# Optimization experiments

Measured on AMD Instinct MI355X. Metric: run time of the kernel, lower is better.

Reference implementation:

```python
import jax, jax.numpy as jnp
import numpy as np

B, S, DM, H, DF = 2, 2048, 1024, 16, 4096
HD = DM // H
EPS = 1e-6
NEG = -1e9


def setup_inputs() -> dict:
    key = jax.random.key(0)
    ks = jax.random.split(key, 16)
    sc = 1.0 / np.sqrt(DM)
    scf = 1.0 / np.sqrt(DF)
    return {
        "x": jax.random.normal(ks[0], (B, S, DM), jnp.float32),
        "src_mask": jax.random.randint(ks[1], (B, 1, 1, S), 0, 2, jnp.int32),
        "Wq": jax.random.normal(ks[2], (DM, DM), jnp.float32) * sc,
        "bq": jnp.zeros((DM,), jnp.float32),
        "Wk": jax.random.normal(ks[3], (DM, DM), jnp.float32) * sc,
        "bk": jnp.zeros((DM,), jnp.float32),
        "Wv": jax.random.normal(ks[4], (DM, DM), jnp.float32) * sc,
        "bv": jnp.zeros((DM,), jnp.float32),
        "Wo": jax.random.normal(ks[5], (DM, DM), jnp.float32) * sc,
        "bo": jnp.zeros((DM,), jnp.float32),
        "W1": jax.random.normal(ks[6], (DM, DF), jnp.float32) * sc,
        "b1": jnp.zeros((DF,), jnp.float32),
        "W2": jax.random.normal(ks[7], (DF, DM), jnp.float32) * scf,
        "b2": jnp.zeros((DM,), jnp.float32),
        "alpha1": jnp.ones((1,), jnp.float32),
        "beta1": jnp.ones((1,), jnp.float32),
        "alpha2": jnp.ones((1,), jnp.float32),
        "beta2": jnp.ones((1,), jnp.float32),
    }


def layer_norm(x, alpha, beta):
    # torch: mean + unbiased std (ddof=1), scalar alpha/beta, eps added to std
    mean = jnp.mean(x, axis=-1, keepdims=True)
    std = jnp.std(x, axis=-1, keepdims=True, ddof=1)
    return alpha * (x - mean) / (std + EPS) + beta


def mha(x, mask, Wq, bq, Wk, bk, Wv, bv, Wo, bo):
    def split(t):  # [B,S,DM] -> [B,H,S,HD]
        return t.reshape(B, S, H, HD).transpose(0, 2, 1, 3)
    q = split(x @ Wq + bq)
    k = split(x @ Wk + bk)
    v = split(x @ Wv + bv)
    scores = jnp.einsum("bhqd,bhkd->bhqk", q, k) / np.sqrt(HD)
    scores = jnp.where(mask == 0, NEG, scores)
    probs = jax.nn.softmax(scores, axis=-1)  # dropout in eval mode = identity
    out = jnp.einsum("bhqk,bhkd->bhqd", probs, v)
    out = out.transpose(0, 2, 1, 3).reshape(B, S, DM)
    return out @ Wo + bo


def reference(x, src_mask, Wq, bq, Wk, bk, Wv, bv, Wo, bo, W1, b1, W2, b2,
              alpha1, beta1, alpha2, beta2):
    # pre-norm residual: x + attn(norm(x)); dropout disabled (eval)
    n1 = layer_norm(x, alpha1, beta1)
    h = x + mha(n1, src_mask, Wq, bq, Wk, bk, Wv, bv, Wo, bo)
    n2 = layer_norm(h, alpha2, beta2)
    ff = jax.nn.relu(n2 @ W1 + b1) @ W2 + b2
    return h + ff
```

## Files before the change

### kernel.cpp

```cpp
#include <hip/hip_runtime.h>
#include <hip/hip_bf16.h>

#define SEQ   2048
#define BATCH 2
#define DMODEL 1024
#define DFF   4096
#define NHEAD 16
#define HDIM  64
#define NTOK  (BATCH*SEQ)

typedef short s8v __attribute__((ext_vector_type(8)));
typedef float f4v __attribute__((ext_vector_type(4)));

__device__ __forceinline__ float b2f(unsigned short u) {
    union { unsigned int i; float f; } v; v.i = ((unsigned int)u) << 16; return v.f;
}
__device__ __forceinline__ unsigned short f2b(float f) {
    union { unsigned int i; float f; } v; v.f = f;
    unsigned int r = v.i + 0x7FFFu + ((v.i >> 16) & 1u);
    return (unsigned short)(r >> 16);
}
__device__ __forceinline__ ushort2 cvt_pk(float a, float b) {
    __hip_bfloat162 h = __float22bfloat162_rn(float2{ a, b });
    return *(ushort2*)&h;
}

__device__ __forceinline__ f4v mfma_bf16(s8v a, s8v b, f4v c) {
    return __builtin_amdgcn_mfma_f32_16x16x32_bf16(a, b, c, 0, 0, 0);
}

__device__ __forceinline__ void gload_lds16(const void* g, void* l) {
    __builtin_amdgcn_global_load_lds(
        (const __attribute__((address_space(1))) unsigned int*)g,
        (__attribute__((address_space(3))) unsigned int*)l, 16, 0, 0);
}

template<int N> __device__ __forceinline__ void wait_vmcnt() {
    if constexpr (N == 8)      asm volatile("s_waitcnt vmcnt(8)" ::: "memory");
    else if constexpr (N == 6) asm volatile("s_waitcnt vmcnt(6)" ::: "memory");
    else if constexpr (N == 2) asm volatile("s_waitcnt vmcnt(2)" ::: "memory");
    else                       asm volatile("s_waitcnt vmcnt(0)" ::: "memory");
}

__device__ __forceinline__ void tp_tile(const float* __restrict__ src,
                                        unsigned short* __restrict__ dst,
                                        int R, int C, int br, int bc, int t,
                                        unsigned short* tl) {
    for (int i = 0; i < 16; i++) {
        int idx = t + 256 * i;
        int r = idx >> 6, c = idx & 63;
        tl[r * 65 + c] = f2b(src[(size_t)(br * 64 + r) * C + bc * 64 + c]);
    }
    __syncthreads();
    for (int i = 0; i < 16; i++) {
        int idx = t + 256 * i;
        int r2 = idx >> 6, c2 = idx & 63;
        dst[(size_t)(bc * 64 + r2) * R + br * 64 + c2] = tl[c2 * 65 + r2];
    }
}

__global__ __launch_bounds__(256) void prep_weights(const float* __restrict__ Wq,
                                                    const float* __restrict__ Wk,
                                                    const float* __restrict__ Wv,
                                                    const float* __restrict__ Wo,
                                                    const float* __restrict__ W1,
                                                    const float* __restrict__ W2,
                                                    const float* __restrict__ bq,
                                                    const float* __restrict__ bk,
                                                    const float* __restrict__ bv,
                                                    const float* __restrict__ x,
                                                    const float* __restrict__ a1,
                                                    const float* __restrict__ be1,
                                                    unsigned short* __restrict__ Wqkv_t,
                                                    unsigned short* __restrict__ Wo_t,
                                                    unsigned short* __restrict__ W1_t,
                                                    unsigned short* __restrict__ W2_t,
                                                    float* __restrict__ bqkv,
                                                    unsigned short* __restrict__ n1) {
    __shared__ unsigned short tl[64 * 65];
    __shared__ float red[8];
    const int t = threadIdx.x;
    const int bx = blockIdx.x, by = blockIdx.y, z = blockIdx.z;
    if (z < 4) {
        const float* src = (z == 0) ? Wq : (z == 1) ? Wk : (z == 2) ? Wv : Wo;
        unsigned short* dst = (z == 3) ? Wo_t : Wqkv_t + (size_t)z * 1024 * 1024;
        tp_tile(src, dst, 1024, 1024, bx, by, t, tl);
    } else if (z == 4) {
        for (int i = 0; i < 4; i++) {
            tp_tile(W1, W1_t, 1024, 4096, bx, by + 16 * i, t, tl);
            __syncthreads();
        }
    } else if (z == 5) {
        if (bx == 0 && by == 0) {
            for (int i = 0; i < 12; i++) {
                int idx = t + 256 * i;
                if (idx < 1024) bqkv[idx] = bq[idx];
                else if (idx < 2048) bqkv[idx] = bk[idx - 1024];
                else if (idx < 3072) bqkv[idx] = bv[idx - 2048];
            }
        }
        for (int i = 0; i < 4; i++) {
            tp_tile(W2, W2_t, 4096, 1024, bx + 16 * i, by, t, tl);
            __syncthreads();
        }
    } else {
        const int row = (z - 6) * 256 + by * 16 + bx;
        const float* xr = x + (size_t)row * DMODEL;
        float4 u = ((const float4*)xr)[t];
        float v[4] = { u.x, u.y, u.z, u.w };
        float s = v[0] + v[1] + v[2] + v[3];
        float sq = v[0]*v[0] + v[1]*v[1] + v[2]*v[2] + v[3]*v[3];
        for (int off = 32; off; off >>= 1) { s += __shfl_xor(s, off); sq += __shfl_xor(sq, off); }
        int wave = t >> 6, lane = t & 63;
        if (!lane) { red[wave] = s; red[4 + wave] = sq; }
        __syncthreads();
        s = red[0] + red[1] + red[2] + red[3];
        sq = red[4] + red[5] + red[6] + red[7];
        float mean = s * (1.f / DMODEL);
        float var = (sq - (float)DMODEL * mean * mean) * (1.f / (DMODEL - 1));
        var = var < 0.f ? 0.f : var;
        float inv = a1[0] / (sqrtf(var) + 1e-6f);
        float bt = be1[0];
        uint2 ou;
        unsigned short r0 = f2b((v[0] - mean) * inv + bt);
        unsigned short r1 = f2b((v[1] - mean) * inv + bt);
        unsigned short r2 = f2b((v[2] - mean) * inv + bt);
        unsigned short r3 = f2b((v[3] - mean) * inv + bt);
        ou.x = (unsigned int)r0 | ((unsigned int)r1 << 16);
        ou.y = (unsigned int)r2 | ((unsigned int)r3 << 16);
        ((uint2*)(n1 + (size_t)row * DMODEL))[t] = ou;
    }
}

__global__ __launch_bounds__(256) void mask_scan(const int* __restrict__ msk,
                                                 int* __restrict__ idx,
                                                 float* __restrict__ maskc2,
                                                 int* __restrict__ ntiles) {
    const int b = blockIdx.x, t = threadIdx.x;
    const int base = b * SEQ;
    __shared__ int wsum[4];
    int k[8]; int cnt = 0;
    for (int j = 0; j < 8; j++) {
        k[j] = (msk[base + t * 8 + j] != 0) ? 1 : 0;
        cnt += k[j];
    }
    const int lane = t & 63, wv = t >> 6;
    int pre = cnt;
    for (int off = 1; off < 64; off <<= 1) {
        int n = __shfl_up(pre, off);
        if (lane >= off) pre += n;
    }
    if (lane == 63) wsum[wv] = pre;
    __syncthreads();
    const int Nb = wsum[0] + wsum[1] + wsum[2] + wsum[3];
    int woff = 0;
    for (int w = 0; w < wv; w++) woff += wsum[w];
    const int excl = woff + pre - cnt;
    for (int j = 0; j < 8; j++) {
        int g = t * 8 + j;
        idx[base + g] = 0;
        maskc2[base + g] = (g < Nb) ? 0.f : -1e9f;
    }
    __syncthreads();
    int pos = excl;
    for (int j = 0; j < 8; j++) {
        if (k[j]) { idx[base + pos] = t * 8 + j; pos++; }
    }
    if (t == 0) ntiles[b] = (Nb + 63) >> 6;
}

__global__ __launch_bounds__(256) void pack_kv(const unsigned short* __restrict__ Kb,
                                               const unsigned short* __restrict__ Vb,
                                               const int* __restrict__ idx,
                                               const int* __restrict__ ntiles,
                                               unsigned short* __restrict__ Kc,
                                               unsigned short* __restrict__ Vc) {
    __shared__ unsigned short tl[64 * 65];
    const int t = threadIdx.x;
    const int kt = blockIdx.x, h = blockIdx.y, b = blockIdx.z;
    if (kt >= ntiles[b]) return;
    const int* idxb = idx + b * SEQ + kt * 64;
    const unsigned short* srcK = Kb + (size_t)b * SEQ * 1024 + h * HDIM;
    unsigned short* dstK = Kc + ((size_t)((b * NHEAD + h) * 32 + kt)) * 4096;
    for (int i = 0; i < 2; i++) {
        int ci = t + 256 * i;
        int r = ci >> 3, cp = ci & 7;
        int cl = cp ^ (r & 7);
        int row = idxb[r];
        *(uint4*)&dstK[ci * 8] = *(const uint4*)&srcK[(size_t)row * 1024 + cl * 8];
    }
    const unsigned short* srcV = Vb + (size_t)b * SEQ * 1024 + h * HDIM;
    for (int i = 0; i < 16; i++) {
        int idx2 = t + 256 * i;
        int r = idx2 >> 6, c = idx2 & 63;
        int row = idxb[r];
        tl[r * 65 + c] = srcV[(size_t)row * 1024 + c];
    }
    __syncthreads();
    unsigned short* dstV = Vc + ((size_t)((b * NHEAD + h) * 32 + kt)) * 4096;
    for (int i = 0; i < 2; i++) {
        int ci = t + 256 * i;
        int r = ci >> 3, cp = ci & 7;
        int cl = cp ^ (r & 7);
        ushort4 e0, e1;
        e0.x = tl[(cl * 8 + 0) * 65 + r]; e0.y = tl[(cl * 8 + 1) * 65 + r];
        e0.z = tl[(cl * 8 + 2) * 65 + r]; e0.w = tl[(cl * 8 + 3) * 65 + r];
        e1.x = tl[(cl * 8 + 4) * 65 + r]; e1.y = tl[(cl * 8 + 5) * 65 + r];
        e1.z = tl[(cl * 8 + 6) * 65 + r]; e1.w = tl[(cl * 8 + 7) * 65 + r];
        *(ushort4*)&dstV[ci * 8]     = e0;
        *(ushort4*)&dstV[ci * 8 + 4] = e1;
    }
}

__global__ __launch_bounds__(256) void ln_kernel(const float* __restrict__ x,
                                                 const float* __restrict__ al,
                                                 const float* __restrict__ be,
                                                 unsigned short* __restrict__ o) {
    const int row = blockIdx.x;
    const float* xr = x + (size_t)row * DMODEL;
    float4 u = ((const float4*)xr)[threadIdx.x];
    float v[4] = { u.x, u.y, u.z, u.w };
    float s = v[0] + v[1] + v[2] + v[3];
    float sq = v[0]*v[0] + v[1]*v[1] + v[2]*v[2] + v[3]*v[3];
    for (int off = 32; off; off >>= 1) { s += __shfl_xor(s, off); sq += __shfl_xor(sq, off); }
    __shared__ float red[8];
    int wave = threadIdx.x >> 6, lane = threadIdx.x & 63;
    if (!lane) { red[wave] = s; red[4 + wave] = sq; }
    __syncthreads();
    s = red[0] + red[1] + red[2] + red[3];
    sq = red[4] + red[5] + red[6] + red[7];
    float mean = s * (1.f / DMODEL);
    float var = (sq - (float)DMODEL * mean * mean) * (1.f / (DMODEL - 1));
    var = var < 0.f ? 0.f : var;
    float inv = al[0] / (sqrtf(var) + 1e-6f);
    float bt = be[0];
    uint2 ou;
    unsigned short r0 = f2b((v[0] - mean) * inv + bt);
    unsigned short r1 = f2b((v[1] - mean) * inv + bt);
    unsigned short r2 = f2b((v[2] - mean) * inv + bt);
    unsigned short r3 = f2b((v[3] - mean) * inv + bt);
    ou.x = (unsigned int)r0 | ((unsigned int)r1 << 16);
    ou.y = (unsigned int)r2 | ((unsigned int)r3 << 16);
    ((uint2*)(o + (size_t)row * DMODEL))[threadIdx.x] = ou;
}

template<int BROWS>
__device__ __forceinline__ void stage256(const unsigned short* __restrict__ A,
                                         const unsigned short* __restrict__ Bt,
                                         int m0, int n0, int K, int k0,
                                         unsigned short* sA, unsigned short* sB, int t) {
#pragma unroll
    for (int i = 0; i < 4; i++) {
        int ci = i * 512 + t;
        int r = ci >> 3, c = (ci & 7) ^ (r & 7);
        gload_lds16(A + (size_t)(m0 + r) * K + k0 + c * 8, sA + (size_t)ci * 8);
    }
#pragma unroll
    for (int i = 0; i < BROWS / 64; i++) {
        int ci = i * 512 + t;
        int r = ci >> 3, c = (ci & 7) ^ (r & 7);
        gload_lds16(Bt + (size_t)(n0 + r) * K + k0 + c * 8, sB + (size_t)ci * 8);
    }
}

template<int NFC>
__device__ __forceinline__ void comp256(const unsigned short* sA, const unsigned short* sB,
                                        int wm, int wn, int l16, int quad,
                                        f4v acc[8][NFC]) {
#pragma unroll
    for (int s = 0; s < 2; s++) {
        s8v b[NFC];
#pragma unroll
        for (int ni = 0; ni < NFC; ni++) {
            int r = wn * (NFC * 16) + ni * 16 + l16;
            int p = (s * 4 + quad) ^ (r & 7);
            b[ni] = *(const s8v*)&sB[r * 64 + p * 8];
        }
#pragma unroll
        for (int mi = 0; mi < 8; mi++) {
            int r = wm * 128 + mi * 16 + l16;
            int p = (s * 4 + quad) ^ (r & 7);
            s8v a = *(const s8v*)&sA[r * 64 + p * 8];
#pragma unroll
            for (int ni = 0; ni < NFC; ni++)
                acc[mi][ni] = mfma_bf16(a, b[ni], acc[mi][ni]);
        }
    }
}

template<bool RELU, bool RES, typename CT, bool SPLIT3, int BN>
__global__ __launch_bounds__(512, 2) void gemm256(const unsigned short* __restrict__ A,
                                                  const unsigned short* __restrict__ Bt,
                                                  const float* __restrict__ bias,
                                                  const float* __restrict__ res,
                                                  CT* __restrict__ C,
                                                  float* __restrict__ pbuf,
                                                  int M, int N, int K, int KS) {
    constexpr int NFC = BN / 64;
    constexpr int LPT = 4 + BN / 64;
    __shared__ __align__(16) unsigned short smA[2][256 * 64];
    __shared__ __align__(16) unsigned short smB[2][BN * 64];
    const int t = threadIdx.x;
    const int wave = t >> 6, lane = t & 63;
    const int quad = lane >> 4, l16 = lane & 15;
    const int wm = wave >> 2, wn = wave & 3;
    const int m0 = blockIdx.x * 256, n0 = blockIdx.y * BN;
    const int z = blockIdx.z;
    const int kbeg = z * KS;
    const int nt = KS >> 6;

    f4v acc[8][NFC] = {};

    stage256<BN>(A, Bt, m0, n0, K, kbeg,      smA[0], smB[0], t);
    stage256<BN>(A, Bt, m0, n0, K, kbeg + 64, smA[1], smB[1], t);
    wait_vmcnt<LPT>();
    __builtin_amdgcn_s_barrier();

    for (int it = 0; it < nt - 2; ++it) {
        const int cb = it & 1;
        __builtin_amdgcn_s_setprio(1);
        comp256<NFC>(smA[cb], smB[cb], wm, wn, l16, quad, acc);
        __builtin_amdgcn_s_setprio(0);
        asm volatile("s_waitcnt lgkmcnt(0)" ::: "memory");
        __builtin_amdgcn_s_barrier();
        stage256<BN>(A, Bt, m0, n0, K, kbeg + (it + 2) * 64, smA[cb], smB[cb], t);
        wait_vmcnt<LPT>();
        __builtin_amdgcn_s_barrier();
    }
    {
        const int cb = (nt - 2) & 1;
        __builtin_amdgcn_s_setprio(1);
        comp256<NFC>(smA[cb], smB[cb], wm, wn, l16, quad, acc);
        __builtin_amdgcn_s_setprio(0);
        asm volatile("s_waitcnt vmcnt(0)" ::: "memory");
        __builtin_amdgcn_s_barrier();
    }
    {
        const int cb = (nt - 1) & 1;
        __builtin_amdgcn_s_setprio(1);
        comp256<NFC>(smA[cb], smB[cb], wm, wn, l16, quad, acc);
        __builtin_amdgcn_s_setprio(0);
    }

#pragma unroll
    for (int mi = 0; mi < 8; mi++) {
#pragma unroll
        for (int ni = 0; ni < NFC; ni++) {
            const int col = n0 + wn * (NFC * 16) + ni * 16 + l16;
            const int row0 = m0 + wm * 128 + mi * 16 + quad * 4;
            if (z == 0) {
                const float bv = bias[col];
#pragma unroll
                for (int r = 0; r < 4; r++) {
                    float v = acc[mi][ni][r] + bv;
                    if (RELU) v = v > 0.f ? v : 0.f;
                    if (RES) v += res[(size_t)(row0 + r) * N + col];
                    size_t cidx;
                    if constexpr (SPLIT3)
                        cidx = (size_t)(col >> 10) * ((size_t)NTOK * 1024)
                             + (size_t)(row0 + r) * 1024 + (col & 1023);
                    else
                        cidx = (size_t)(row0 + r) * N + col;
                    if constexpr (sizeof(CT) == 2)
                        C[cidx] = f2b(v);
                    else
                        C[cidx] = v;
                }
            } else {
#pragma unroll
                for (int r = 0; r < 4; r++)
                    pbuf[(size_t)(z - 1) * M * N + (size_t)(row0 + r) * N + col]
                        = acc[mi][ni][r];
            }
        }
    }
}

__global__ __launch_bounds__(256) void add_pbuf(float* __restrict__ out,
                                                const float* __restrict__ pbuf) {
    const int i0 = (blockIdx.x * 256 + threadIdx.x) * 8;
    float4 a0 = *(const float4*)&out[i0];
    float4 a1 = *(const float4*)&out[i0 + 4];
    float4 p0 = *(const float4*)&pbuf[i0];
    float4 p1 = *(const float4*)&pbuf[i0 + 4];
    a0.x += p0.x; a0.y += p0.y; a0.z += p0.z; a0.w += p0.w;
    a1.x += p1.x; a1.y += p1.y; a1.z += p1.z; a1.w += p1.w;
    *(float4*)&out[i0]     = a0;
    *(float4*)&out[i0 + 4] = a1;
}

#define EXPC 0.18033688f
__device__ __forceinline__ void attn_tile(const unsigned short* __restrict__ smKb,
                                          const unsigned short* __restrict__ smVb,
                                          const float* __restrict__ smM, int k0,
                                          unsigned short* __restrict__ smPw,
                                          s8v qf0, s8v qf1, int quad, int l16,
                                          float& l_s, f4v* oacc) {
    const int l7 = l16 & 7;
    f4v s[4];
#pragma unroll
    for (int kt4 = 0; kt4 < 4; kt4++) {
        int r = kt4 * 16 + l16;
        s8v kf0 = *(const s8v*)&smKb[r * 64 + ((quad ^ l7) * 8)];
        s8v kf1 = *(const s8v*)&smKb[r * 64 + (((quad + 4) ^ l7) * 8)];
        f4v z = {};
        z = mfma_bf16(kf0, qf0, z);
        z = mfma_bf16(kf1, qf1, z);
        s[kt4] = z;
    }
#pragma unroll
    for (int kt4 = 0; kt4 < 4; kt4++) {
        float4 mf = *(const float4*)&smM[k0 + kt4 * 16 + quad * 4];
        s[kt4][0] = s[kt4][0] * EXPC + mf.x;
        s[kt4][1] = s[kt4][1] * EXPC + mf.y;
        s[kt4][2] = s[kt4][2] * EXPC + mf.z;
        s[kt4][3] = s[kt4][3] * EXPC + mf.w;
    }
#pragma unroll
    for (int kt4 = 0; kt4 < 4; kt4++)
#pragma unroll
        for (int r = 0; r < 4; r++) {
            float p = __builtin_amdgcn_exp2f(s[kt4][r]);
            s[kt4][r] = p;
            l_s += p;
        }
#pragma unroll
    for (int kt4 = 0; kt4 < 4; kt4++) {
        ushort2 p01 = cvt_pk(s[kt4][0], s[kt4][1]);
        ushort2 p23 = cvt_pk(s[kt4][2], s[kt4][3]);
        ushort4 pk;
        pk.x = p01.x; pk.y = p01.y; pk.z = p23.x; pk.w = p23.y;
        int c = kt4 * 2 + (quad >> 1);
        *(ushort4*)&smPw[l16 * 64 + ((c ^ l7) * 8 + (quad & 1) * 4)] = pk;
    }
    s8v pf0 = *(const s8v*)&smPw[l16 * 64 + ((quad ^ l7) * 8)];
    s8v pf1 = *(const s8v*)&smPw[l16 * 64 + (((quad + 4) ^ l7) * 8)];
#pragma unroll
    for (int nt = 0; nt < 4; nt++) {
        int r = nt * 16 + l16;
        s8v v0 = *(const s8v*)&smVb[r * 64 + ((quad ^ l7) * 8)];
        s8v v1 = *(const s8v*)&smVb[r * 64 + (((quad + 4) ^ l7) * 8)];
        oacc[nt] = mfma_bf16(pf0, v0, oacc[nt]);
        oacc[nt] = mfma_bf16(pf1, v1, oacc[nt]);
    }
}

__global__ __launch_bounds__(512) void attn_kernel(const unsigned short* __restrict__ Qb,
                                                   const unsigned short* __restrict__ Kc,
                                                   const unsigned short* __restrict__ Vc,
                                                   const float* __restrict__ maskc2,
                                                   const int* __restrict__ ntiles,
                                                   unsigned short* __restrict__ out) {
    __shared__ __align__(16) unsigned short smK[2][4096];
    __shared__ __align__(16) unsigned short smV[2][4096];
    __shared__ __align__(16) unsigned short smP[8][1024];
    __shared__ __align__(16) float smM[SEQ];

    const int t = threadIdx.x;
    const int wave = t >> 6, lane = t & 63;
    const int quad = lane >> 4, l16 = lane & 15;
    const int qt = blockIdx.x, h = blockIdx.y, b = blockIdx.z;
    const int q0 = qt * 128 + wave * 16;
    const int nt = ntiles[b];
    const unsigned short* Kbh = Kc + ((size_t)(b * NHEAD + h)) * 32 * 4096;
    const unsigned short* Vbh = Vc + ((size_t)(b * NHEAD + h)) * 32 * 4096;
    unsigned short* smPw = &smP[wave][0];

    const unsigned short* Qp = Qb + ((size_t)b * SEQ + q0 + l16) * 1024 + h * HDIM + quad * 8;
    s8v qf0 = *(const s8v*)(Qp);
    s8v qf1 = *(const s8v*)(Qp + 32);

    gload_lds16(maskc2 + (size_t)b * SEQ + t * 4, (float*)smM + t * 4);
    gload_lds16(Kbh + t * 8,        smK[0] + t * 8);
    gload_lds16(Vbh + t * 8,        smV[0] + t * 8);
    gload_lds16(Kbh + 4096 + t * 8, smK[1] + t * 8);
    gload_lds16(Vbh + 4096 + t * 8, smV[1] + t * 8);
    wait_vmcnt<2>();
    __builtin_amdgcn_s_barrier();

    float l_s = 0.f;
    f4v oacc[4] = {};

    for (int it = 0; it < nt; ++it) {
        const int cb = it & 1;
        __builtin_amdgcn_s_setprio(1);
        attn_tile(smK[cb], smV[cb], smM, it * 64, smPw, qf0, qf1, quad, l16, l_s, oacc);
        __builtin_amdgcn_s_setprio(0);
        if (it + 2 < nt) {
            asm volatile("s_waitcnt lgkmcnt(0)" ::: "memory");
            __builtin_amdgcn_s_barrier();
            gload_lds16(Kbh + (size_t)(it + 2) * 4096 + t * 8, smK[cb] + t * 8);
            gload_lds16(Vbh + (size_t)(it + 2) * 4096 + t * 8, smV[cb] + t * 8);
            wait_vmcnt<2>();
            __builtin_amdgcn_s_barrier();
        } else if (it + 1 < nt) {
            asm volatile("s_waitcnt lgkmcnt(0)" ::: "memory");
            __builtin_amdgcn_s_barrier();
            wait_vmcnt<0>();
            __builtin_amdgcn_s_barrier();
        }
    }

    l_s += __shfl_xor(l_s, 16);
    l_s += __shfl_xor(l_s, 32);
    float lrr[4];
    for (int r = 0; r < 4; r++) lrr[r] = __shfl(l_s, quad * 4 + r);
    for (int nt2 = 0; nt2 < 4; nt2++)
        for (int r = 0; r < 4; r++) {
            int row = q0 + quad * 4 + r;
            int col = h * HDIM + nt2 * 16 + l16;
            out[((size_t)b * SEQ + row) * DMODEL + col] = f2b(oacc[nt2][r] / lrr[r]);
        }
}

extern "C" void kernel_launch(void* const* d_in, const int* in_sizes, int n_in,
                              void* d_out, int out_size, void* d_ws, size_t ws_size,
                              hipStream_t stream) {
    const float* x   = (const float*)d_in[0];
    const int*   msk = (const int*)d_in[1];
    const float* Wq  = (const float*)d_in[2];
    const float* bq  = (const float*)d_in[3];
    const float* Wk  = (const float*)d_in[4];
    const float* bk  = (const float*)d_in[5];
    const float* Wv  = (const float*)d_in[6];
    const float* bv  = (const float*)d_in[7];
    const float* Wo  = (const float*)d_in[8];
    const float* bo  = (const float*)d_in[9];
    const float* W1  = (const float*)d_in[10];
    const float* b1  = (const float*)d_in[11];
    const float* W2  = (const float*)d_in[12];
    const float* b2  = (const float*)d_in[13];
    const float* a1  = (const float*)d_in[14];
    const float* be1 = (const float*)d_in[15];
    const float* a2  = (const float*)d_in[16];
    const float* be2 = (const float*)d_in[17];
    float* outf = (float*)d_out;

    char* ws = (char*)d_ws;
    const size_t MB = 1024 * 1024;
    unsigned short* W2_t   = (unsigned short*)(ws);
    unsigned short* W1_t   = (unsigned short*)(ws + 8 * MB);
    float*          Pbuf   = (float*)(ws + 8 * MB);
    unsigned short* Wqkv_t = (unsigned short*)(ws + 16 * MB);
    float*          bqkv   = (float*)(ws + 22 * MB);
    unsigned short* Kc     = (unsigned short*)(ws + 16 * MB);
    unsigned short* n2     = (unsigned short*)(ws + 16 * MB);
    unsigned short* Wo_t   = (unsigned short*)(ws + 24 * MB);
    unsigned short* Qb     = (unsigned short*)(ws + 26 * MB);
    unsigned short* Kb     = (unsigned short*)(ws + 34 * MB);
    unsigned short* Vb     = (unsigned short*)(ws + 42 * MB);
    float*          Pbuf2  = (float*)(ws + 34 * MB);
    unsigned short* ff1    = (unsigned short*)(ws + 26 * MB);
    unsigned short* attnO  = (unsigned short*)(ws + 50 * MB);
    unsigned short* n1     = (unsigned short*)d_out;
    unsigned short* Vc     = (unsigned short*)d_out;
    float*          hbuf   = (float*)d_out;
    float*          maskc2 = (float*)((char*)d_out + 8 * MB);
    int*            idxc   = (int*)((char*)d_out + 8 * MB + 16 * 1024);
    int*            ntl    = (int*)((char*)d_out + 8 * MB + 32 * 1024);

    mask_scan<<<dim3(BATCH), 256, 0, stream>>>(msk, idxc, maskc2, ntl);
    prep_weights<<<dim3(16, 16, 22), 256, 0, stream>>>(
        Wq, Wk, Wv, Wo, W1, W2, bq, bk, bv, x, a1, be1,
        Wqkv_t, Wo_t, W1_t, W2_t, bqkv, n1);

    gemm256<false, false, unsigned short, true, 256><<<dim3(16, 12, 1), 512, 0, stream>>>(
        n1, Wqkv_t, bqkv, nullptr, Qb, nullptr, NTOK, 3072, 1024, 1024);
    pack_kv<<<dim3(32, 16, 2), 256, 0, stream>>>(Kb, Vb, idxc, ntl, Kc, Vc);
    attn_kernel<<<dim3(16, 16, 2), 512, 0, stream>>>(Qb, Kc, Vc, maskc2, ntl, attnO);
    gemm256<false, true, float, false, 128><<<dim3(16, 8, 2), 512, 0, stream>>>(
        attnO, Wo_t, bo, x, hbuf, Pbuf2, NTOK, 1024, 1024, 512);
    add_pbuf<<<dim3(2048), 256, 0, stream>>>(hbuf, Pbuf2);
    ln_kernel<<<NTOK, 256, 0, stream>>>(hbuf, a2, be2, n2);
    gemm256<true, false, unsigned short, false, 256><<<dim3(16, 16, 1), 512, 0, stream>>>(
        n2, W1_t, b1, nullptr, ff1, nullptr, NTOK, DFF, 1024, 1024);
    gemm256<false, true, float, false, 128><<<dim3(16, 8, 2), 512, 0, stream>>>(
        ff1, W2_t, b2, hbuf, outf, Pbuf, NTOK, 1024, 4096, 2048);
    add_pbuf<<<dim3(2048), 256, 0, stream>>>(outf, Pbuf);
}
```

Measured before the change: 353.1 us.

## Replace 256-row GEMMs with 128x128 intra-K-split kernel and fuse small launches

Replaces the 256-row GEMM with a 128x128-tile kernel in which two wave groups split each K-step and reduce their partial sums through LDS. Block order is swizzled for cache locality, and the attention grid is swizzled the same way. Mask scanning moves into the prep kernel and the split-K partial add merges into LayerNorm, cutting launches. Transpose tiles now use vectorized float4 loads and ushort4 stores. Smaller tiles raise occupancy and the block count, but lower per-tile data reuse and add an LDS reduction.

```diff
diff --git a/kernel.cpp b/kernel.cpp
--- a/kernel.cpp
+++ b/kernel.cpp
@@ -38,6 +38,7 @@
 template<int N> __device__ __forceinline__ void wait_vmcnt() {
     if constexpr (N == 8)      asm volatile("s_waitcnt vmcnt(8)" ::: "memory");
     else if constexpr (N == 6) asm volatile("s_waitcnt vmcnt(6)" ::: "memory");
+    else if constexpr (N == 4) asm volatile("s_waitcnt vmcnt(4)" ::: "memory");
     else if constexpr (N == 2) asm volatile("s_waitcnt vmcnt(2)" ::: "memory");
     else                       asm volatile("s_waitcnt vmcnt(0)" ::: "memory");
 }
@@ -46,16 +47,25 @@
                                         unsigned short* __restrict__ dst,
                                         int R, int C, int br, int bc, int t,
                                         unsigned short* tl) {
-    for (int i = 0; i < 16; i++) {
-        int idx = t + 256 * i;
-        int r = idx >> 6, c = idx & 63;
-        tl[r * 65 + c] = f2b(src[(size_t)(br * 64 + r) * C + bc * 64 + c]);
+    for (int i = 0; i < 4; i++) {
+        int lin = i * 1024 + t * 4;
+        int r = lin >> 6, c = lin & 63;
+        float4 u = *(const float4*)&src[(size_t)(br * 64 + r) * C + bc * 64 + c];
+        tl[r * 65 + c + 0] = f2b(u.x);
+        tl[r * 65 + c + 1] = f2b(u.y);
+        tl[r * 65 + c + 2] = f2b(u.z);
+        tl[r * 65 + c + 3] = f2b(u.w);
     }
     __syncthreads();
-    for (int i = 0; i < 16; i++) {
-        int idx = t + 256 * i;
-        int r2 = idx >> 6, c2 = idx & 63;
-        dst[(size_t)(bc * 64 + r2) * R + br * 64 + c2] = tl[c2 * 65 + r2];
+    for (int i = 0; i < 4; i++) {
+        int lin = i * 1024 + t * 4;
+        int r2 = lin >> 6, c2 = lin & 63;
+        ushort4 o;
+        o.x = tl[(c2 + 0) * 65 + r2];
+        o.y = tl[(c2 + 1) * 65 + r2];
+        o.z = tl[(c2 + 2) * 65 + r2];
+        o.w = tl[(c2 + 3) * 65 + r2];
+        *(ushort4*)&dst[(size_t)(bc * 64 + r2) * R + br * 64 + c2] = o;
     }
 }
 
@@ -71,14 +81,19 @@
                                                     const float* __restrict__ x,
                                                     const float* __restrict__ a1,
                                                     const float* __restrict__ be1,
+                                                    const int* __restrict__ msk,
                                                     unsigned short* __restrict__ Wqkv_t,
                                                     unsigned short* __restrict__ Wo_t,
                                                     unsigned short* __restrict__ W1_t,
                                                     unsigned short* __restrict__ W2_t,
                                                     float* __restrict__ bqkv,
-                                                    unsigned short* __restrict__ n1) {
+                                                    unsigned short* __restrict__ n1,
+                                                    int* __restrict__ idxc,
+                                                    float* __restrict__ maskc2,
+                                                    int* __restrict__ ntl) {
     __shared__ unsigned short tl[64 * 65];
     __shared__ float red[8];
+    __shared__ int wsum[4];
     const int t = threadIdx.x;
     const int bx = blockIdx.x, by = blockIdx.y, z = blockIdx.z;
     if (z < 4) {
@@ -103,6 +118,38 @@
             tp_tile(W2, W2_t, 4096, 1024, bx + 16 * i, by, t, tl);
             __syncthreads();
         }
+    } else if (z == 22) {
+        if (bx >= BATCH || by != 0) return;
+        const int b = bx;
+        const int base = b * SEQ;
+        int k[8]; int cnt = 0;
+        for (int j = 0; j < 8; j++) {
+            k[j] = (msk[base + t * 8 + j] != 0) ? 1 : 0;
+            cnt += k[j];
+        }
+        const int lane = t & 63, wv = t >> 6;
+        int pre = cnt;
+        for (int off = 1; off < 64; off <<= 1) {
+            int n = __shfl_up(pre, off);
+            if (lane >= off) pre += n;
+        }
+        if (lane == 63) wsum[wv] = pre;
+        __syncthreads();
+        const int Nb = wsum[0] + wsum[1] + wsum[2] + wsum[3];
+        int woff = 0;
+        for (int w = 0; w < wv; w++) woff += wsum[w];
+        const int excl = woff + pre - cnt;
+        for (int j = 0; j < 8; j++) {
+            int g = t * 8 + j;
+            idxc[base + g] = 0;
+            maskc2[base + g] = (g < Nb) ? 0.f : -1e9f;
+        }
+        __syncthreads();
+        int pos = excl;
+        for (int j = 0; j < 8; j++) {
+            if (k[j]) { idxc[base + pos] = t * 8 + j; pos++; }
+        }
+        if (t == 0) ntl[b] = (Nb + 63) >> 6;
     } else {
         const int row = (z - 6) * 256 + by * 16 + bx;
         const float* xr = x + (size_t)row * DMODEL;
@@ -132,43 +179,6 @@
     }
 }
 
-__global__ __launch_bounds__(256) void mask_scan(const int* __restrict__ msk,
-                                                 int* __restrict__ idx,
-                                                 float* __restrict__ maskc2,
-                                                 int* __restrict__ ntiles) {
-    const int b = blockIdx.x, t = threadIdx.x;
-    const int base = b * SEQ;
-    __shared__ int wsum[4];
-    int k[8]; int cnt = 0;
-    for (int j = 0; j < 8; j++) {
-        k[j] = (msk[base + t * 8 + j] != 0) ? 1 : 0;
-        cnt += k[j];
-    }
-    const int lane = t & 63, wv = t >> 6;
-    int pre = cnt;
-    for (int off = 1; off < 64; off <<= 1) {
-        int n = __shfl_up(pre, off);
-        if (lane >= off) pre += n;
-    }
-    if (lane == 63) wsum[wv] = pre;
-    __syncthreads();
-    const int Nb = wsum[0] + wsum[1] + wsum[2] + wsum[3];
-    int woff = 0;
-    for (int w = 0; w < wv; w++) woff += wsum[w];
-    const int excl = woff + pre - cnt;
-    for (int j = 0; j < 8; j++) {
-        int g = t * 8 + j;
-        idx[base + g] = 0;
-        maskc2[base + g] = (g < Nb) ? 0.f : -1e9f;
-    }
-    __syncthreads();
-    int pos = excl;
-    for (int j = 0; j < 8; j++) {
-        if (k[j]) { idx[base + pos] = t * 8 + j; pos++; }
-    }
-    if (t == 0) ntiles[b] = (Nb + 63) >> 6;
-}
-
 __global__ __launch_bounds__(256) void pack_kv(const unsigned short* __restrict__ Kb,
                                                const unsigned short* __restrict__ Vb,
                                                const int* __restrict__ idx,
@@ -212,13 +222,18 @@
     }
 }
 
-__global__ __launch_bounds__(256) void ln_kernel(const float* __restrict__ x,
-                                                 const float* __restrict__ al,
-                                                 const float* __restrict__ be,
-                                                 unsigned short* __restrict__ o) {
+__global__ __launch_bounds__(256) void ln_add(float* __restrict__ hb,
+                                              const float* __restrict__ pbuf,
+                                              const float* __restrict__ al,
+                                              const float* __restrict__ be,
+                                              unsigned short* __restrict__ o) {
     const int row = blockIdx.x;
-    const float* xr = x + (size_t)row * DMODEL;
-    float4 u = ((const float4*)xr)[threadIdx.x];
+    float* hr = hb + (size_t)row * DMODEL;
+    const float* pr = pbuf + (size_t)row * DMODEL;
+    float4 u = ((const float4*)hr)[threadIdx.x];
+    float4 p = ((const float4*)pr)[threadIdx.x];
+    u.x += p.x; u.y += p.y; u.z += p.z; u.w += p.w;
+    ((float4*)hr)[threadIdx.x] = u;
     float v[4] = { u.x, u.y, u.z, u.w };
     float s = v[0] + v[1] + v[2] + v[3];
     float sq = v[0]*v[0] + v[1]*v[1] + v[2]*v[2] + v[3]*v[3];
@@ -244,138 +259,6 @@
     ((uint2*)(o + (size_t)row * DMODEL))[threadIdx.x] = ou;
 }
 
-template<int BROWS>
-__device__ __forceinline__ void stage256(const unsigned short* __restrict__ A,
-                                         const unsigned short* __restrict__ Bt,
-                                         int m0, int n0, int K, int k0,
-                                         unsigned short* sA, unsigned short* sB, int t) {
-#pragma unroll
-    for (int i = 0; i < 4; i++) {
-        int ci = i * 512 + t;
-        int r = ci >> 3, c = (ci & 7) ^ (r & 7);
-        gload_lds16(A + (size_t)(m0 + r) * K + k0 + c * 8, sA + (size_t)ci * 8);
-    }
-#pragma unroll
-    for (int i = 0; i < BROWS / 64; i++) {
-        int ci = i * 512 + t;
-        int r = ci >> 3, c = (ci & 7) ^ (r & 7);
-        gload_lds16(Bt + (size_t)(n0 + r) * K + k0 + c * 8, sB + (size_t)ci * 8);
-    }
-}
-
-template<int NFC>
-__device__ __forceinline__ void comp256(const unsigned short* sA, const unsigned short* sB,
-                                        int wm, int wn, int l16, int quad,
-                                        f4v acc[8][NFC]) {
-#pragma unroll
-    for (int s = 0; s < 2; s++) {
-        s8v b[NFC];
-#pragma unroll
-        for (int ni = 0; ni < NFC; ni++) {
-            int r = wn * (NFC * 16) + ni * 16 + l16;
-            int p = (s * 4 + quad) ^ (r & 7);
-            b[ni] = *(const s8v*)&sB[r * 64 + p * 8];
-        }
-#pragma unroll
-        for (int mi = 0; mi < 8; mi++) {
-            int r = wm * 128 + mi * 16 + l16;
-            int p = (s * 4 + quad) ^ (r & 7);
-            s8v a = *(const s8v*)&sA[r * 64 + p * 8];
-#pragma unroll
-            for (int ni = 0; ni < NFC; ni++)
-                acc[mi][ni] = mfma_bf16(a, b[ni], acc[mi][ni]);
-        }
-    }
-}
-
-template<bool RELU, bool RES, typename CT, bool SPLIT3, int BN>
-__global__ __launch_bounds__(512, 2) void gemm256(const unsigned short* __restrict__ A,
-                                                  const unsigned short* __restrict__ Bt,
-                                                  const float* __restrict__ bias,
-                                                  const float* __restrict__ res,
-                                                  CT* __restrict__ C,
-                                                  float* __restrict__ pbuf,
-                                                  int M, int N, int K, int KS) {
-    constexpr int NFC = BN / 64;
-    constexpr int LPT = 4 + BN / 64;
-    __shared__ __align__(16) unsigned short smA[2][256 * 64];
-    __shared__ __align__(16) unsigned short smB[2][BN * 64];
-    const int t = threadIdx.x;
-    const int wave = t >> 6, lane = t & 63;
-    const int quad = lane >> 4, l16 = lane & 15;
-    const int wm = wave >> 2, wn = wave & 3;
-    const int m0 = blockIdx.x * 256, n0 = blockIdx.y * BN;
-    const int z = blockIdx.z;
-    const int kbeg = z * KS;
-    const int nt = KS >> 6;
-
-    f4v acc[8][NFC] = {};
-
-    stage256<BN>(A, Bt, m0, n0, K, kbeg,      smA[0], smB[0], t);
-    stage256<BN>(A, Bt, m0, n0, K, kbeg + 64, smA[1], smB[1], t);
-    wait_vmcnt<LPT>();
-    __builtin_amdgcn_s_barrier();
-
-    for (int it = 0; it < nt - 2; ++it) {
-        const int cb = it & 1;
-        __builtin_amdgcn_s_setprio(1);
-        comp256<NFC>(smA[cb], smB[cb], wm, wn, l16, quad, acc);
-        __builtin_amdgcn_s_setprio(0);
-        asm volatile("s_waitcnt lgkmcnt(0)" ::: "memory");
-        __builtin_amdgcn_s_barrier();
-        stage256<BN>(A, Bt, m0, n0, K, kbeg + (it + 2) * 64, smA[cb], smB[cb], t);
-        wait_vmcnt<LPT>();
-        __builtin_amdgcn_s_barrier();
-    }
-    {
-        const int cb = (nt - 2) & 1;
-        __builtin_amdgcn_s_setprio(1);
-        comp256<NFC>(smA[cb], smB[cb], wm, wn, l16, quad, acc);
-        __builtin_amdgcn_s_setprio(0);
-        asm volatile("s_waitcnt vmcnt(0)" ::: "memory");
-        __builtin_amdgcn_s_barrier();
-    }
-    {
-        const int cb = (nt - 1) & 1;
-        __builtin_amdgcn_s_setprio(1);
-        comp256<NFC>(smA[cb], smB[cb], wm, wn, l16, quad, acc);
-        __builtin_amdgcn_s_setprio(0);
-    }
-
-#pragma unroll
-    for (int mi = 0; mi < 8; mi++) {
-#pragma unroll
-        for (int ni = 0; ni < NFC; ni++) {
-            const int col = n0 + wn * (NFC * 16) + ni * 16 + l16;
-            const int row0 = m0 + wm * 128 + mi * 16 + quad * 4;
-            if (z == 0) {
-                const float bv = bias[col];
-#pragma unroll
-                for (int r = 0; r < 4; r++) {
-                    float v = acc[mi][ni][r] + bv;
-                    if (RELU) v = v > 0.f ? v : 0.f;
-                    if (RES) v += res[(size_t)(row0 + r) * N + col];
-                    size_t cidx;
-                    if constexpr (SPLIT3)
-                        cidx = (size_t)(col >> 10) * ((size_t)NTOK * 1024)
-                             + (size_t)(row0 + r) * 1024 + (col & 1023);
-                    else
-                        cidx = (size_t)(row0 + r) * N + col;
-                    if constexpr (sizeof(CT) == 2)
-                        C[cidx] = f2b(v);
-                    else
-                        C[cidx] = v;
-                }
-            } else {
-#pragma unroll
-                for (int r = 0; r < 4; r++)
-                    pbuf[(size_t)(z - 1) * M * N + (size_t)(row0 + r) * N + col]
-                        = acc[mi][ni][r];
-            }
-        }
-    }
-}
-
 __global__ __launch_bounds__(256) void add_pbuf(float* __restrict__ out,
                                                 const float* __restrict__ pbuf) {
     const int i0 = (blockIdx.x * 256 + threadIdx.x) * 8;
@@ -389,6 +272,141 @@
     *(float4*)&out[i0 + 4] = a1;
 }
 
+
+__device__ __forceinline__ void stage128(const unsigned short* __restrict__ mat,
+                                         int base, int K, int k0,
+                                         unsigned short* sdst, int t) {
+#pragma unroll
+    for (int q = 0; q < 2; q++) {
+        int rl = t >> 3;
+        int c  = (t & 7) ^ (rl & 7);
+        gload_lds16(mat + (size_t)(base + q * 64 + rl) * K + k0 + c * 8,
+                    sdst + q * 4096 + (size_t)t * 8);
+    }
+}
+
+__device__ __forceinline__ s8v rdfrag128(const unsigned short* sm, int q, int fi,
+                                         int l16, int quad, int sW) {
+    int rl = fi * 16 + l16;
+    int p = (sW * 4 + quad) ^ (l16 & 7);
+    return *(const s8v*)&sm[q * 4096 + rl * 64 + p * 8];
+}
+
+template<bool RELU, bool RES, bool SPLITK, bool SPLIT3, typename CT>
+__global__ __launch_bounds__(512, 4) void gemm128k(const unsigned short* __restrict__ A,
+                                                   const unsigned short* __restrict__ Bt,
+                                                   const float* __restrict__ bias,
+                                                   const float* __restrict__ res,
+                                                   CT* __restrict__ C,
+                                                   float* __restrict__ pbuf,
+                                                   int M, int N, int K, int KS) {
+    __shared__ __align__(16) unsigned short smem[4][8192];
+    const int t = threadIdx.x;
+    const int wave = t >> 6, lane = t & 63;
+    const int quad = lane >> 4, l16 = lane & 15;
+    const int sW = wave >> 2, wm = (wave >> 1) & 1, wn = wave & 1;
+    const int lin = blockIdx.x + blockIdx.y * gridDim.x;
+    const int cpx = (gridDim.x * gridDim.y) >> 3;
+    const int swz = (lin & 7) * cpx + (lin >> 3);
+    int z, m0, n0;
+    if constexpr (SPLITK) {
+        z  = swz & 1;
+        m0 = ((swz >> 1) & 31) * 128;
+        n0 = (swz >> 6) * 128;
+    } else {
+        z  = 0;
+        m0 = (swz & 31) * 128;
+        n0 = (swz >> 5) * 128;
+    }
+    const int kbeg = z * KS;
+    const int nt = KS >> 6;
+
+    f4v acc[4][4] = {};
+
+    stage128(A,  m0, K, kbeg,      smem[0], t);
+    stage128(Bt, n0, K, kbeg,      smem[2], t);
+    stage128(A,  m0, K, kbeg + 64, smem[1], t);
+    stage128(Bt, n0, K, kbeg + 64, smem[3], t);
+    wait_vmcnt<4>();
+    __builtin_amdgcn_s_barrier();
+
+    for (int it = 0; it < nt; ++it) {
+        const int cb = it & 1;
+        const unsigned short* sA = smem[cb];
+        const unsigned short* sB = smem[2 + cb];
+        s8v a[4], b[4];
+#pragma unroll
+        for (int i = 0; i < 4; i++) a[i] = rdfrag128(sA, wm, i, l16, quad, sW);
+#pragma unroll
+        for (int i = 0; i < 4; i++) b[i] = rdfrag128(sB, wn, i, l16, quad, sW);
+        __builtin_amdgcn_s_setprio(1);
+#pragma unroll
+        for (int mi = 0; mi < 4; mi++)
+#pragma unroll
+            for (int ni = 0; ni < 4; ni++)
+                acc[mi][ni] = mfma_bf16(a[mi], b[ni], acc[mi][ni]);
+        __builtin_amdgcn_s_setprio(0);
+        asm volatile("s_waitcnt lgkmcnt(0)" ::: "memory");
+        __builtin_amdgcn_s_barrier();
+        if (it + 2 < nt) {
+            stage128(A,  m0, K, kbeg + (it + 2) * 64, smem[cb], t);
+            stage128(Bt, n0, K, kbeg + (it + 2) * 64, smem[2 + cb], t);
+            wait_vmcnt<4>();
+        } else if (it + 1 < nt) {
+            wait_vmcnt<0>();
+        }
+        __builtin_amdgcn_s_barrier();
+    }
+
+    float* xch = (float*)&smem[0][0];
+    float* myx = xch + (wm * 2 + wn) * 4096;
+    if (sW == 1) {
+#pragma unroll
+        for (int mi = 0; mi < 4; mi++)
+#pragma unroll
+            for (int ni = 0; ni < 4; ni++)
+                *(f4v*)&myx[(mi * 4 + ni) * 256 + lane * 4] = acc[mi][ni];
+    }
+    __builtin_amdgcn_s_barrier();
+    if (sW == 0) {
+#pragma unroll
+        for (int mi = 0; mi < 4; mi++)
+#pragma unroll
+            for (int ni = 0; ni < 4; ni++)
+                acc[mi][ni] += *(const f4v*)&myx[(mi * 4 + ni) * 256 + lane * 4];
+#pragma unroll
+        for (int mi = 0; mi < 4; mi++)
+#pragma unroll
+            for (int ni = 0; ni < 4; ni++) {
+                const int col = n0 + wn * 64 + ni * 16 + l16;
+                const int row0 = m0 + wm * 64 + mi * 16 + quad * 4;
+                if (!SPLITK || z == 0) {
+                    const float bv = bias[col];
+#pragma unroll
+                    for (int r = 0; r < 4; r++) {
+                        float v = acc[mi][ni][r] + bv;
+                        if (RELU) v = v > 0.f ? v : 0.f;
+                        if (RES) v += res[(size_t)(row0 + r) * N + col];
+                        size_t ix;
+                        if constexpr (SPLIT3)
+                            ix = (size_t)(col >> 10) * ((size_t)NTOK * 1024)
+                               + (size_t)(row0 + r) * 1024 + (col & 1023);
+                        else
+                            ix = (size_t)(row0 + r) * N + col;
+                        if constexpr (sizeof(CT) == 2)
+                            C[ix] = f2b(v);
+                        else
+                            C[ix] = v;
+                    }
+                } else {
+#pragma unroll
+                    for (int r = 0; r < 4; r++)
+                        pbuf[(size_t)(row0 + r) * N + col] = acc[mi][ni][r];
+                }
+            }
+    }
+}
+
 #define EXPC 0.18033688f
 __device__ __forceinline__ void attn_tile(const unsigned short* __restrict__ smKb,
                                           const unsigned short* __restrict__ smVb,
@@ -459,7 +477,9 @@
     const int t = threadIdx.x;
     const int wave = t >> 6, lane = t & 63;
     const int quad = lane >> 4, l16 = lane & 15;
-    const int qt = blockIdx.x, h = blockIdx.y, b = blockIdx.z;
+    const int lin = blockIdx.x + (blockIdx.y << 4) + (blockIdx.z << 8);
+    const int swz = (lin & 7) * 64 + (lin >> 3);
+    const int qt = swz & 15, h = (swz >> 4) & 15, b = swz >> 8;
     const int q0 = qt * 128 + wave * 16;
     const int nt = ntiles[b];
     const unsigned short* Kbh = Kc + ((size_t)(b * NHEAD + h)) * 32 * 4096;
@@ -559,22 +579,20 @@
     int*            idxc   = (int*)((char*)d_out + 8 * MB + 16 * 1024);
     int*            ntl    = (int*)((char*)d_out + 8 * MB + 32 * 1024);
 
-    mask_scan<<<dim3(BATCH), 256, 0, stream>>>(msk, idxc, maskc2, ntl);
-    prep_weights<<<dim3(16, 16, 22), 256, 0, stream>>>(
-        Wq, Wk, Wv, Wo, W1, W2, bq, bk, bv, x, a1, be1,
-        Wqkv_t, Wo_t, W1_t, W2_t, bqkv, n1);
-
-    gemm256<false, false, unsigned short, true, 256><<<dim3(16, 12, 1), 512, 0, stream>>>(
+    prep_weights<<<dim3(16, 16, 23), 256, 0, stream>>>(
+        Wq, Wk, Wv, Wo, W1, W2, bq, bk, bv, x, a1, be1, msk,
+        Wqkv_t, Wo_t, W1_t, W2_t, bqkv, n1, idxc, maskc2, ntl);
+
+    gemm128k<false, false, false, true, unsigned short><<<dim3(32, 24), 512, 0, stream>>>(
         n1, Wqkv_t, bqkv, nullptr, Qb, nullptr, NTOK, 3072, 1024, 1024);
     pack_kv<<<dim3(32, 16, 2), 256, 0, stream>>>(Kb, Vb, idxc, ntl, Kc, Vc);
     attn_kernel<<<dim3(16, 16, 2), 512, 0, stream>>>(Qb, Kc, Vc, maskc2, ntl, attnO);
-    gemm256<false, true, float, false, 128><<<dim3(16, 8, 2), 512, 0, stream>>>(
+    gemm128k<false, true, true, false, float><<<dim3(64, 8), 512, 0, stream>>>(
         attnO, Wo_t, bo, x, hbuf, Pbuf2, NTOK, 1024, 1024, 512);
-    add_pbuf<<<dim3(2048), 256, 0, stream>>>(hbuf, Pbuf2);
-    ln_kernel<<<NTOK, 256, 0, stream>>>(hbuf, a2, be2, n2);
-    gemm256<true, false, unsigned short, false, 256><<<dim3(16, 16, 1), 512, 0, stream>>>(
-        n2, W1_t, b1, nullptr, ff1, nullptr, NTOK, DFF, 1024, 1024);
-    gemm256<false, true, float, false, 128><<<dim3(16, 8, 2), 512, 0, stream>>>(
+    ln_add<<<NTOK, 256, 0, stream>>>(hbuf, Pbuf2, a2, be2, n2);
+    gemm128k<true, false, false, false, unsigned short><<<dim3(32, 32), 512, 0, stream>>>(
+        n2, W1_t, b1, nullptr, ff1, nullptr, NTOK, 4096, 1024, 1024);
+    gemm128k<false, true, true, false, float><<<dim3(64, 8), 512, 0, stream>>>(
         ff1, W2_t, b2, hbuf, outf, Pbuf, NTOK, 1024, 4096, 2048);
     add_pbuf<<<dim3(2048), 256, 0, stream>>>(outf, Pbuf);
 }
```

Result: no change. 347.2 us (-1.7%).
